# Kernel tuning notes

Measured on AMD Instinct MI355X. Metric: run time of the kernel, lower is better.

Reference implementation:

```python
import jax, jax.numpy as jnp
import numpy as np

B, S, D, H = 2, 2048, 1024, 16
DK = D // H


def setup_inputs() -> dict:
    key = jax.random.key(0)
    ks = jax.random.split(key, 12)
    scale = 1.0 / np.sqrt(D)
    inp = {
        "query": jax.random.normal(ks[0], (B, S, D), jnp.float32),
        "key": jax.random.normal(ks[1], (B, S, D), jnp.float32),
        "value": jax.random.normal(ks[2], (B, S, D), jnp.float32),
        "mask": jax.random.randint(ks[3], (B, 1, S, S), 0, 2, jnp.int32),
        "Wq": jax.random.normal(ks[4], (D, D), jnp.float32) * scale,
        "bq": jnp.zeros((D,), jnp.float32),
        "Wk": jax.random.normal(ks[5], (D, D), jnp.float32) * scale,
        "bk": jnp.zeros((D,), jnp.float32),
        "Wv": jax.random.normal(ks[6], (D, D), jnp.float32) * scale,
        "bv": jnp.zeros((D,), jnp.float32),
        "Wo": jax.random.normal(ks[7], (D, D), jnp.float32) * scale,
        "bo": jnp.zeros((D,), jnp.float32),
    }
    return inp


def reference(query, key, value, mask, Wq, bq, Wk, bk, Wv, bv, Wo, bo):
    # Linear projections (dropout is identity in eval mode)
    q = query @ Wq + bq          # (B,S,D)
    k = key @ Wk + bk
    v = value @ Wv + bv

    # split heads: (B,S,D) -> (B,H,S,DK)
    def split(x):
        return x.reshape(B, S, H, DK).transpose(0, 2, 1, 3)

    q, k, v = split(q), split(k), split(v)

    scores = jnp.einsum("bhqd,bhkd->bhqk", q, k) / jnp.sqrt(jnp.float32(DK))
    scores = jnp.where(mask == 0, jnp.float32(-1e9), scores)
    p_attn = jax.nn.softmax(scores, axis=-1)   # (B,H,S,S)

    att = jnp.einsum("bhqk,bhkd->bhqd", p_attn, v)  # (B,H,S,DK)
    merged = att.transpose(0, 2, 1, 3).reshape(B, S, D)
    return merged @ Wo + bo
```

## Files before the change

### kernel.cpp

```cpp
#include <hip/hip_runtime.h>
#include <hip/hip_bf16.h>
#include <cstdint>
#include <cstddef>


#define B_ 2
#define S_ 2048
#define D_ 1024
#define H_ 16
#define M_ 4096

typedef unsigned short u16;
typedef __attribute__((ext_vector_type(8))) short bf16x8;
typedef __attribute__((ext_vector_type(8))) unsigned short u16x8;
typedef __attribute__((ext_vector_type(4))) unsigned short u16x4;
typedef __attribute__((ext_vector_type(4))) unsigned int u32x4;
typedef __attribute__((ext_vector_type(4))) float f32x4;
typedef __attribute__((ext_vector_type(4))) int i32x4;

#define QSCALE 0.18033688011112042f

__device__ __forceinline__ u16 f2bf(float f) {
  __hip_bfloat16 h = __float2bfloat16(f);
  return *reinterpret_cast<u16*>(&h);
}

__device__ __forceinline__ unsigned cvtpk(float lo, float hi) {
  unsigned r;
  asm("v_cvt_pk_bf16_f32 %0, %1, %2" : "=v"(r) : "v"(lo), "v"(hi));
  return r;
}

__device__ __forceinline__ void gload_lds16(const void* g, void* l) {
  __builtin_amdgcn_global_load_lds((const __attribute__((address_space(1))) void*)g,
                                   (__attribute__((address_space(3))) void*)l, 16, 0, 0);
}

__global__ __launch_bounds__(256) void k_prep(const float* __restrict__ q, const float* __restrict__ k,
                                              const float* __restrict__ v,
                                              u16* __restrict__ xq, u16* __restrict__ xk, u16* __restrict__ xv,
                                              const float* __restrict__ w0, const float* __restrict__ w1,
                                              const float* __restrict__ w2, const float* __restrict__ w3,
                                              u16* __restrict__ t0, u16* __restrict__ t1,
                                              u16* __restrict__ t2, u16* __restrict__ t3,
                                              const int* __restrict__ mask, u16* __restrict__ mout) {
  __shared__ float tile[32][33];
  const int id = blockIdx.x;
  const int tid = threadIdx.x;
  if (id < 6144) {
    const int z = id >> 11;
    const int bx = id & 2047;
    const float* src = (z == 0) ? q : (z == 1) ? k : v;
    u16* dst = (z == 0) ? xq : (z == 1) ? xk : xv;
    size_t i = ((size_t)bx * 256 + tid) * 8;
    f32x4 a = *(const f32x4*)(src + i);
    f32x4 b = *(const f32x4*)(src + i + 4);
    u16x8 o;
    o[0]=f2bf(a[0]); o[1]=f2bf(a[1]); o[2]=f2bf(a[2]); o[3]=f2bf(a[3]);
    o[4]=f2bf(b[0]); o[5]=f2bf(b[1]); o[6]=f2bf(b[2]); o[7]=f2bf(b[3]);
    *(u16x8*)(dst + i) = o;
  } else if (id < 10240) {
    const int id2 = id - 6144;
    const int z = id2 >> 10;
    const int rem = id2 & 1023;
    const int bx0 = (rem & 31) * 32, by0 = (rem >> 5) * 32;
    const float* W = (z==0)?w0:(z==1)?w1:(z==2)?w2:w3;
    u16* Wt = (z==0)?t0:(z==1)?t1:(z==2)?t2:t3;
    int tx = tid & 31, ty = tid >> 5;
    #pragma unroll
    for (int p = 0; p < 4; ++p)
      tile[ty + p*8][tx] = W[(size_t)(by0 + ty + p*8) * D_ + bx0 + tx];
    __syncthreads();
    #pragma unroll
    for (int p = 0; p < 4; ++p)
      Wt[(size_t)(bx0 + ty + p*8) * D_ + by0 + tx] = f2bf(tile[tx][ty + p*8]);
  } else {
    size_t tt = (size_t)(id - 10240) * 256 + tid;
    const int* p = mask + tt * 64;
    unsigned wds0 = 0, wds1 = 0, wds2 = 0, wds3 = 0;
    #pragma unroll
    for (int c = 0; c < 16; ++c) {
      i32x4 vv = *(const i32x4*)(p + c*4);
      #pragma unroll
      for (int e = 0; e < 4; ++e) {
        const int kk = c*4 + e;
        const int lcw = (kk >> 3) & 3;
        const int ni = ((kk >> 4) & 2) | ((kk >> 2) & 1);
        const unsigned bit = 1u << (4*ni + (kk & 3));
        if (vv[e]) {
          if (lcw == 0) wds0 |= bit; else if (lcw == 1) wds1 |= bit;
          else if (lcw == 2) wds2 |= bit; else wds3 |= bit;
        }
      }
    }
    u16x4 w; w[0] = (u16)wds0; w[1] = (u16)wds1; w[2] = (u16)wds2; w[3] = (u16)wds3;
    *(u16x4*)(mout + tt*4) = w;
  }
}

template<int CMODE, int MI, int NI>
__device__ __forceinline__ void gemm_core(const u16* __restrict__ A, const u16* __restrict__ Bt,
                                          const float* __restrict__ bias, void* __restrict__ Cv, float scale) {
  extern __shared__ u16 sm[];
  constexpr int ASZ = MI*32*64;
  u16* As = sm;
  u16* Bs = sm + ASZ;
  const int t = threadIdx.x;
  const int l = t & 63, w = t >> 6;
  const int wr = w >> 1, wc = w & 1;
  const int lr = l & 15, lc = l >> 4;
  const int bm = blockIdx.x, bn = blockIdx.y;
  f32x4 acc[MI][NI];
  #pragma unroll
  for (int i = 0; i < MI; ++i)
    #pragma unroll
    for (int j = 0; j < NI; ++j) { f32x4 z = {0.f,0.f,0.f,0.f}; acc[i][j] = z; }
  const int srow = t >> 3;
  const int blkx = (t & 7) ^ (srow & 7);
  const u16* ga = A  + (size_t)(bm*(MI*32) + srow)*1024 + blkx*8;
  const u16* gb = Bt + (size_t)(bn*(NI*32) + srow)*1024 + blkx*8;
  for (int kt = 0; kt < 16; ++kt) {
    const int ko = kt * 64;
    __syncthreads();
    #pragma unroll
    for (int i = 0; i < MI; ++i)
      gload_lds16(ga + (size_t)(i*32)*1024 + ko, &As[i*2048 + t*8]);
    #pragma unroll
    for (int i = 0; i < NI; ++i)
      gload_lds16(gb + (size_t)(i*32)*1024 + ko, &Bs[i*2048 + t*8]);
    __syncthreads();
    #pragma unroll
    for (int ks = 0; ks < 2; ++ks) {
      bf16x8 af[MI], bfr[NI];
      #pragma unroll
      for (int mi = 0; mi < MI; ++mi)
        af[mi]  = *(const bf16x8*)&As[(wr*(MI*16) + mi*16 + lr)*64 + (((ks*4 + lc) ^ (lr & 7))*8)];
      #pragma unroll
      for (int ni = 0; ni < NI; ++ni)
        bfr[ni] = *(const bf16x8*)&Bs[(wc*(NI*16) + ni*16 + lr)*64 + (((ks*4 + lc) ^ (lr & 7))*8)];
      #pragma unroll
      for (int mi = 0; mi < MI; ++mi)
        #pragma unroll
        for (int ni = 0; ni < NI; ++ni)
          acc[mi][ni] = __builtin_amdgcn_mfma_f32_16x16x32_bf16(af[mi], bfr[ni], acc[mi][ni], 0, 0, 0);
    }
  }
  #pragma unroll
  for (int ni = 0; ni < NI; ++ni) {
    int gcol = bn*(NI*32) + wc*(NI*16) + ni*16 + lr;
    float bv = bias[gcol];
    #pragma unroll
    for (int mi = 0; mi < MI; ++mi) {
      int grow = bm*(MI*32) + wr*(MI*16) + mi*16 + lc*4;
      if (CMODE == 2) {
        u16x4 pk;
        #pragma unroll
        for (int j = 0; j < 4; ++j) pk[j] = f2bf((acc[mi][ni][j] + bv) * scale);
        *(u16x4*)&((u16*)Cv)[(size_t)gcol * M_ + grow] = pk;
      } else {
        #pragma unroll
        for (int j = 0; j < 4; ++j) {
          float v = (acc[mi][ni][j] + bv) * scale;
          if (CMODE == 0) ((u16*)Cv)[(size_t)(grow + j) * 1024 + gcol] = f2bf(v);
          else            ((float*)Cv)[(size_t)(grow + j) * 1024 + gcol] = v;
        }
      }
    }
  }
}

__global__ __launch_bounds__(256, 4) void k_gemm_qkv(const u16* Xq, const u16* Xk, const u16* Xv,
                                                     const u16* Wqt, const u16* Wkt, const u16* Wvt,
                                                     const float* bq, const float* bk, const float* bv,
                                                     u16* Qo, u16* Ko, u16* Vt, float qscale) {
  int z = blockIdx.z;
  if (z == 0)      gemm_core<0,4,4>(Xq, Wqt, bq, Qo, qscale);
  else if (z == 1) gemm_core<0,4,4>(Xk, Wkt, bk, Ko, 1.f);
  else             gemm_core<2,4,4>(Xv, Wvt, bv, Vt, 1.f);
}

__global__ __launch_bounds__(256, 4) void k_gemm_out(const u16* Aatt, const u16* Wot, const float* bo, float* out) {
  gemm_core<1,4,2>(Aatt, Wot, bo, out, 1.f);
}

__global__ __launch_bounds__(512, 4) void k_attn(const u16* __restrict__ Q, const u16* __restrict__ Kb,
                                                 const u16* __restrict__ Vt,
                                                 const u16* __restrict__ mbw,
                                                 u16* __restrict__ attb) {
  __shared__ u16 Ks[4*4096];
  __shared__ u16 Vs[4*4096];
  const int t = threadIdx.x, l = t & 63, w = t >> 6;
  const int lr = l & 15, lc = l >> 4;
  const int id = blockIdx.x + (blockIdx.y << 4) + (blockIdx.z << 8);
  const int lg = (id & 7) * 64 + (id >> 3);
  const int qt = lg & 15, h = (lg >> 4) & 15, b = lg >> 8;
  const int r0 = t >> 3;
  const int c0 = (t & 7) ^ (r0 & 7);
  const int pr0 = (r0 & 32) | ((r0 & 12) << 1) | ((r0 & 16) >> 2) | (r0 & 3);
  const u16* kp0 = Kb + (size_t)(b*S_ + pr0)*D_ + h*64 + c0*8;
  const u16* vp0 = Vt + (size_t)(h*64 + r0)*M_ + b*S_ + c0*8;

  gload_lds16(Q + (size_t)(b*S_ + qt*128 + r0)*D_      + h*64 + c0*8, &Ks[t*8]);
  gload_lds16(Q + (size_t)(b*S_ + qt*128 + 64 + r0)*D_ + h*64 + c0*8, &Ks[4096 + t*8]);
  __syncthreads();
  const int qrow = w*16 + lr;
  const int sw0 = ((lc     ) ^ (lr & 7)) * 8;
  const int sw1 = ((4 + lc ) ^ (lr & 7)) * 8;
  const int qbuf = (qrow >> 6) * 4096, qrl = (qrow & 63) * 64;
  bf16x8 aq0 = *(const bf16x8*)&Ks[qbuf + qrl + sw0];
  bf16x8 aq1 = *(const bf16x8*)&Ks[qbuf + qrl + sw1];
  __syncthreads();
  gload_lds16(kp0,                  &Ks[t*8]);
  gload_lds16(vp0,                  &Vs[t*8]);
  gload_lds16(kp0 + (size_t)64*D_,  &Ks[4096 + t*8]);
  gload_lds16(vp0 + 64,             &Vs[4096 + t*8]);

  const short one_bf = (short)0x3F80;
  const bf16x8 onesf = {one_bf,one_bf,one_bf,one_bf,one_bf,one_bf,one_bf,one_bf};
  f32x4 ls = {0.f,0.f,0.f,0.f};
  f32x4 o[4];
  #pragma unroll
  for (int ni = 0; ni < 4; ++ni) { f32x4 z = {0.f,0.f,0.f,0.f}; o[ni] = z; }
  const u16* mkp = mbw + (size_t)(b*S_ + qt*128 + qrow)*128 + lc;
  const u16* kpp = kp0;
  const u16* vpp = vp0;

#define ATILE(MN, SL) {                                                                \
    unsigned mw = mkp[(MN)*4];                                                         \
    f32x4 s[4];                                                                        \
    _Pragma("unroll")                                                                  \
    for (int ni = 0; ni < 4; ++ni) { f32x4 z = {0.f,0.f,0.f,0.f}; s[ni] = z; }         \
    __builtin_amdgcn_s_setprio(1);                                                     \
    _Pragma("unroll")                                                                  \
    for (int ni = 0; ni < 4; ++ni) {                                                   \
      bf16x8 bk0 = *(const bf16x8*)&Ks[(SL)*4096 + (ni*16 + lr)*64 + sw0];             \
      bf16x8 bk1 = *(const bf16x8*)&Ks[(SL)*4096 + (ni*16 + lr)*64 + sw1];             \
      s[ni] = __builtin_amdgcn_mfma_f32_16x16x32_bf16(bk0, aq0, s[ni], 0, 0, 0);       \
      s[ni] = __builtin_amdgcn_mfma_f32_16x16x32_bf16(bk1, aq1, s[ni], 0, 0, 0);       \
    }                                                                                  \
    __builtin_amdgcn_s_setprio(0);                                                     \
    _Pragma("unroll")                                                                  \
    for (int ni = 0; ni < 4; ++ni)                                                     \
      _Pragma("unroll")                                                                \
      for (int j = 0; j < 4; ++j) {                                                    \
        float pv = __builtin_amdgcn_exp2f(s[ni][j]);                                   \
        int bmsk = ((int)(mw << (31 - (4*ni + j)))) >> 31;                             \
        union { float f; int i; } u; u.f = pv; u.i &= bmsk;                            \
        s[ni][j] = u.f;                                                                \
      }                                                                                \
    u32x4 pw0, pw1;                                                                    \
    pw0[0] = cvtpk(s[0][0], s[0][1]); pw0[1] = cvtpk(s[0][2], s[0][3]);                \
    pw0[2] = cvtpk(s[1][0], s[1][1]); pw0[3] = cvtpk(s[1][2], s[1][3]);                \
    pw1[0] = cvtpk(s[2][0], s[2][1]); pw1[1] = cvtpk(s[2][2], s[2][3]);                \
    pw1[2] = cvtpk(s[3][0], s[3][1]); pw1[3] = cvtpk(s[3][2], s[3][3]);                \
    bf16x8 pa0 = __builtin_bit_cast(bf16x8, pw0);                                      \
    bf16x8 pa1 = __builtin_bit_cast(bf16x8, pw1);                                      \
    __builtin_amdgcn_s_setprio(1);                                                     \
    ls = __builtin_amdgcn_mfma_f32_16x16x32_bf16(pa0, onesf, ls, 0, 0, 0);             \
    ls = __builtin_amdgcn_mfma_f32_16x16x32_bf16(pa1, onesf, ls, 0, 0, 0);             \
    _Pragma("unroll")                                                                  \
    for (int ni = 0; ni < 4; ++ni) {                                                   \
      bf16x8 bv0 = *(const bf16x8*)&Vs[(SL)*4096 + (ni*16 + lr)*64 + sw0];             \
      o[ni] = __builtin_amdgcn_mfma_f32_16x16x32_bf16(pa0, bv0, o[ni], 0, 0, 0);       \
    }                                                                                  \
    _Pragma("unroll")                                                                  \
    for (int ni = 0; ni < 4; ++ni) {                                                   \
      bf16x8 bv1 = *(const bf16x8*)&Vs[(SL)*4096 + (ni*16 + lr)*64 + sw1];             \
      o[ni] = __builtin_amdgcn_mfma_f32_16x16x32_bf16(pa1, bv1, o[ni], 0, 0, 0);       \
    }                                                                                  \
    __builtin_amdgcn_s_setprio(0);                                                     \
  }

#define APHASE(PC, PRE) {                                                              \
    __syncthreads();                                                                   \
    if (PRE) {                                                                         \
      gload_lds16(kpp + (size_t)2*64*D_, &Ks[((1-(PC))*2    )*4096 + t*8]);            \
      gload_lds16(vpp + 2*64,            &Vs[((1-(PC))*2    )*4096 + t*8]);            \
      gload_lds16(kpp + (size_t)3*64*D_, &Ks[((1-(PC))*2 + 1)*4096 + t*8]);            \
      gload_lds16(vpp + 3*64,            &Vs[((1-(PC))*2 + 1)*4096 + t*8]);            \
    }                                                                                  \
    ATILE(0, (PC)*2);                                                                  \
    ATILE(1, (PC)*2 + 1);                                                              \
    kpp += (size_t)2*64*D_; vpp += 2*64; mkp += 8;                                     \
  }

  for (int it = 0; it < 7; ++it) {
    APHASE(0, 1)
    APHASE(1, 1)
  }
  APHASE(0, 1)
  APHASE(1, 0)
#undef APHASE
#undef ATILE

  float rl[4];
  #pragma unroll
  for (int j = 0; j < 4; ++j) rl[j] = 1.f / ls[j];
  #pragma unroll
  for (int ni = 0; ni < 4; ++ni)
    #pragma unroll
    for (int j = 0; j < 4; ++j) {
      int orow = qt*128 + w*16 + lc*4 + j, dcol = ni*16 + lr;
      attb[(size_t)(b*S_ + orow)*D_ + h*64 + dcol] = f2bf(o[ni][j] * rl[j]);
    }
}

extern "C" void kernel_launch(void* const* d_in, const int* in_sizes, int n_in,
                              void* d_out, int out_size, void* d_ws, size_t ws_size,
                              hipStream_t stream) {
  (void)in_sizes; (void)n_in; (void)out_size; (void)ws_size;
  const float* query = (const float*)d_in[0];
  const float* key   = (const float*)d_in[1];
  const float* value = (const float*)d_in[2];
  const int*   mask  = (const int*)d_in[3];
  const float* Wq = (const float*)d_in[4];
  const float* bq = (const float*)d_in[5];
  const float* Wk = (const float*)d_in[6];
  const float* bk = (const float*)d_in[7];
  const float* Wv = (const float*)d_in[8];
  const float* bv = (const float*)d_in[9];
  const float* Wo = (const float*)d_in[10];
  const float* bo = (const float*)d_in[11];
  float* out = (float*)d_out;
  char* ws = (char*)d_ws;
  const size_t MB = 1024 * 1024;
  u16* Xq  = (u16*)(ws + 0*MB);
  u16* Xk  = (u16*)(ws + 8*MB);
  u16* Xv  = (u16*)(ws + 16*MB);
  u16* Wqt = (u16*)(ws + 24*MB);
  u16* Wkt = (u16*)(ws + 26*MB);
  u16* Wvt = (u16*)(ws + 28*MB);
  u16* Wot = (u16*)(ws + 30*MB);
  u16* Qb  = (u16*)(ws + 32*MB);
  u16* Kb  = (u16*)(ws + 40*MB);
  u16* Vtb = (u16*)(ws + 48*MB);
  u16* mbits = (u16*)(ws + 56*MB);
  u16* attb = (u16*)(ws + 0*MB);

  k_prep     <<<dim3(10752),       256, 0,     stream>>>(query, key, value, Xq, Xk, Xv,
                                                         Wq, Wk, Wv, Wo, Wqt, Wkt, Wvt, Wot,
                                                         mask, mbits);
  k_gemm_qkv <<<dim3(32, 8, 3),    256, 32768, stream>>>(Xq, Xk, Xv, Wqt, Wkt, Wvt, bq, bk, bv,
                                                         Qb, Kb, Vtb, QSCALE);
  k_attn     <<<dim3(16, 16, 2),   512, 0,     stream>>>(Qb, Kb, Vtb, mbits, attb);
  k_gemm_out <<<dim3(32, 16),      256, 24576, stream>>>(attb, Wot, bo, out);
}
```

Baseline: 133.3 us.

## Split attention key range across two warp groups with 64-row query tiles

The attention kernel now processes 64 query rows per block instead of 128, doubling the grid. The key dimension is split between two groups of four waves, each handling half the keys in 32-key steps, and the partial outputs and row sums are combined through LDS at the end. The mask bit packing is simplified to a plain 64-bit word per row chunk, read one byte per step. This is meant to raise parallelism and cut per-wave serial latency, at the cost of an LDS reduction, smaller tiles per step and extra barriers.

```diff
diff --git a/kernel.cpp b/kernel.cpp
--- a/kernel.cpp
+++ b/kernel.cpp
@@ -11,6 +11,7 @@
 #define M_ 4096
 
 typedef unsigned short u16;
+typedef unsigned char u8;
 typedef __attribute__((ext_vector_type(8))) short bf16x8;
 typedef __attribute__((ext_vector_type(8))) unsigned short u16x8;
 typedef __attribute__((ext_vector_type(4))) unsigned short u16x4;
@@ -43,7 +44,7 @@
                                               const float* __restrict__ w2, const float* __restrict__ w3,
                                               u16* __restrict__ t0, u16* __restrict__ t1,
                                               u16* __restrict__ t2, u16* __restrict__ t3,
-                                              const int* __restrict__ mask, u16* __restrict__ mout) {
+                                              const int* __restrict__ mask, unsigned long long* __restrict__ mout) {
   __shared__ float tile[32][33];
   const int id = blockIdx.x;
   const int tid = threadIdx.x;
@@ -77,24 +78,15 @@
   } else {
     size_t tt = (size_t)(id - 10240) * 256 + tid;
     const int* p = mask + tt * 64;
-    unsigned wds0 = 0, wds1 = 0, wds2 = 0, wds3 = 0;
+    unsigned long long bits = 0ull;
     #pragma unroll
     for (int c = 0; c < 16; ++c) {
       i32x4 vv = *(const i32x4*)(p + c*4);
       #pragma unroll
-      for (int e = 0; e < 4; ++e) {
-        const int kk = c*4 + e;
-        const int lcw = (kk >> 3) & 3;
-        const int ni = ((kk >> 4) & 2) | ((kk >> 2) & 1);
-        const unsigned bit = 1u << (4*ni + (kk & 3));
-        if (vv[e]) {
-          if (lcw == 0) wds0 |= bit; else if (lcw == 1) wds1 |= bit;
-          else if (lcw == 2) wds2 |= bit; else wds3 |= bit;
-        }
-      }
+      for (int e = 0; e < 4; ++e)
+        if (vv[e]) bits |= 1ull << (c*4 + e);
     }
-    u16x4 w; w[0] = (u16)wds0; w[1] = (u16)wds1; w[2] = (u16)wds2; w[3] = (u16)wds3;
-    *(u16x4*)(mout + tt*4) = w;
+    mout[tt] = bits;
   }
 }
 
@@ -185,35 +177,40 @@
 
 __global__ __launch_bounds__(512, 4) void k_attn(const u16* __restrict__ Q, const u16* __restrict__ Kb,
                                                  const u16* __restrict__ Vt,
-                                                 const u16* __restrict__ mbw,
+                                                 const u8* __restrict__ mbw,
                                                  u16* __restrict__ attb) {
-  __shared__ u16 Ks[4*4096];
-  __shared__ u16 Vs[4*4096];
+  __shared__ u16 smem[16384];
+  u16* Ks = smem;
+  u16* Vs = smem + 8192;
   const int t = threadIdx.x, l = t & 63, w = t >> 6;
   const int lr = l & 15, lc = l >> 4;
-  const int id = blockIdx.x + (blockIdx.y << 4) + (blockIdx.z << 8);
-  const int lg = (id & 7) * 64 + (id >> 3);
-  const int qt = lg & 15, h = (lg >> 4) & 15, b = lg >> 8;
-  const int r0 = t >> 3;
-  const int c0 = (t & 7) ^ (r0 & 7);
-  const int pr0 = (r0 & 32) | ((r0 & 12) << 1) | ((r0 & 16) >> 2) | (r0 & 3);
-  const u16* kp0 = Kb + (size_t)(b*S_ + pr0)*D_ + h*64 + c0*8;
-  const u16* vp0 = Vt + (size_t)(h*64 + r0)*M_ + b*S_ + c0*8;
-
-  gload_lds16(Q + (size_t)(b*S_ + qt*128 + r0)*D_      + h*64 + c0*8, &Ks[t*8]);
-  gload_lds16(Q + (size_t)(b*S_ + qt*128 + 64 + r0)*D_ + h*64 + c0*8, &Ks[4096 + t*8]);
+  const int g = w >> 2;
+  const int wq = w & 3;
+  const int id = blockIdx.x + (blockIdx.y << 5) + (blockIdx.z << 9);
+  const int lg = (id & 7) * 128 + (id >> 3);
+  const int qt = lg & 31, h = (lg >> 5) & 15, b = lg >> 9;
+  const int u = t & 255;
+  const int kr = u >> 3;
+  const int kc = (u & 7) ^ (kr & 7);
+  const int kpr = ((kr & 12) << 1) | ((kr & 16) >> 2) | (kr & 3);
+  const u16* kp = Kb + ((size_t)(b*S_ + g*1024 + kpr))*D_ + h*64 + kc*8;
+  const int vr = u >> 2;
+  const int vc = (u & 3) ^ (vr & 3);
+  const u16* vp = Vt + ((size_t)(h*64 + vr))*M_ + b*S_ + g*1024 + vc*8;
+
+  {
+    int qr = t >> 3, qc = (t & 7) ^ (qr & 7);
+    gload_lds16(Q + (size_t)(b*S_ + qt*64 + qr)*D_ + h*64 + qc*8, &smem[t*8]);
+  }
   __syncthreads();
-  const int qrow = w*16 + lr;
   const int sw0 = ((lc     ) ^ (lr & 7)) * 8;
   const int sw1 = ((4 + lc ) ^ (lr & 7)) * 8;
-  const int qbuf = (qrow >> 6) * 4096, qrl = (qrow & 63) * 64;
-  bf16x8 aq0 = *(const bf16x8*)&Ks[qbuf + qrl + sw0];
-  bf16x8 aq1 = *(const bf16x8*)&Ks[qbuf + qrl + sw1];
+  const int qrow = wq*16 + lr;
+  bf16x8 aq0 = *(const bf16x8*)&smem[qrow*64 + sw0];
+  bf16x8 aq1 = *(const bf16x8*)&smem[qrow*64 + sw1];
   __syncthreads();
-  gload_lds16(kp0,                  &Ks[t*8]);
-  gload_lds16(vp0,                  &Vs[t*8]);
-  gload_lds16(kp0 + (size_t)64*D_,  &Ks[4096 + t*8]);
-  gload_lds16(vp0 + 64,             &Vs[4096 + t*8]);
+  gload_lds16(kp, &Ks[(g*2)*2048 + u*8]);
+  gload_lds16(vp, &Vs[(g*2)*2048 + u*8]);
 
   const short one_bf = (short)0x3F80;
   const bf16x8 onesf = {one_bf,one_bf,one_bf,one_bf,one_bf,one_bf,one_bf,one_bf};
@@ -221,88 +218,95 @@
   f32x4 o[4];
   #pragma unroll
   for (int ni = 0; ni < 4; ++ni) { f32x4 z = {0.f,0.f,0.f,0.f}; o[ni] = z; }
-  const u16* mkp = mbw + (size_t)(b*S_ + qt*128 + qrow)*128 + lc;
-  const u16* kpp = kp0;
-  const u16* vpp = vp0;
-
-#define ATILE(MN, SL) {                                                                \
-    unsigned mw = mkp[(MN)*4];                                                         \
-    f32x4 s[4];                                                                        \
-    _Pragma("unroll")                                                                  \
-    for (int ni = 0; ni < 4; ++ni) { f32x4 z = {0.f,0.f,0.f,0.f}; s[ni] = z; }         \
+  const u16* kpp = kp;
+  const u16* vpp = vp;
+  const u8* mkp = mbw + (size_t)(b*S_ + qt*64 + qrow)*256 + g*128 + lc;
+  const int vsw = (lc ^ (lr & 3)) * 8;
+
+#define APH(P, PRE) {                                                                  \
+    __syncthreads();                                                                   \
+    unsigned mw = (unsigned)(*mkp);                                                    \
+    if (PRE) {                                                                         \
+      gload_lds16(kpp + (size_t)32*D_, &Ks[(g*2 + ((P)^1))*2048 + u*8]);               \
+      gload_lds16(vpp + 32,            &Vs[(g*2 + ((P)^1))*2048 + u*8]);               \
+    }                                                                                  \
+    f32x4 s0 = {0.f,0.f,0.f,0.f}, s1 = {0.f,0.f,0.f,0.f};                              \
     __builtin_amdgcn_s_setprio(1);                                                     \
-    _Pragma("unroll")                                                                  \
-    for (int ni = 0; ni < 4; ++ni) {                                                   \
-      bf16x8 bk0 = *(const bf16x8*)&Ks[(SL)*4096 + (ni*16 + lr)*64 + sw0];             \
-      bf16x8 bk1 = *(const bf16x8*)&Ks[(SL)*4096 + (ni*16 + lr)*64 + sw1];             \
-      s[ni] = __builtin_amdgcn_mfma_f32_16x16x32_bf16(bk0, aq0, s[ni], 0, 0, 0);       \
-      s[ni] = __builtin_amdgcn_mfma_f32_16x16x32_bf16(bk1, aq1, s[ni], 0, 0, 0);       \
+    {                                                                                  \
+      const int kb = (g*2 + (P))*2048;                                                 \
+      bf16x8 bk00 = *(const bf16x8*)&Ks[kb + lr*64 + sw0];                             \
+      bf16x8 bk01 = *(const bf16x8*)&Ks[kb + lr*64 + sw1];                             \
+      bf16x8 bk10 = *(const bf16x8*)&Ks[kb + (16 + lr)*64 + sw0];                      \
+      bf16x8 bk11 = *(const bf16x8*)&Ks[kb + (16 + lr)*64 + sw1];                      \
+      s0 = __builtin_amdgcn_mfma_f32_16x16x32_bf16(bk00, aq0, s0, 0, 0, 0);            \
+      s0 = __builtin_amdgcn_mfma_f32_16x16x32_bf16(bk01, aq1, s0, 0, 0, 0);            \
+      s1 = __builtin_amdgcn_mfma_f32_16x16x32_bf16(bk10, aq0, s1, 0, 0, 0);            \
+      s1 = __builtin_amdgcn_mfma_f32_16x16x32_bf16(bk11, aq1, s1, 0, 0, 0);            \
     }                                                                                  \
     __builtin_amdgcn_s_setprio(0);                                                     \
     _Pragma("unroll")                                                                  \
-    for (int ni = 0; ni < 4; ++ni)                                                     \
+    for (int j = 0; j < 4; ++j) {                                                      \
+      float pv = __builtin_amdgcn_exp2f(s0[j]);                                        \
+      int bm0 = ((int)(mw << (31 - j))) >> 31;                                         \
+      union { float f; int i; } u0; u0.f = pv; u0.i &= bm0; s0[j] = u0.f;              \
+      float pw = __builtin_amdgcn_exp2f(s1[j]);                                        \
+      int bm1 = ((int)(mw << (27 - j))) >> 31;                                         \
+      union { float f; int i; } u1; u1.f = pw; u1.i &= bm1; s1[j] = u1.f;              \
+    }                                                                                  \
+    u32x4 pw4;                                                                         \
+    pw4[0] = cvtpk(s0[0], s0[1]); pw4[1] = cvtpk(s0[2], s0[3]);                        \
+    pw4[2] = cvtpk(s1[0], s1[1]); pw4[3] = cvtpk(s1[2], s1[3]);                        \
+    bf16x8 pa = __builtin_bit_cast(bf16x8, pw4);                                       \
+    __builtin_amdgcn_s_setprio(1);                                                     \
+    ls = __builtin_amdgcn_mfma_f32_16x16x32_bf16(pa, onesf, ls, 0, 0, 0);              \
+    {                                                                                  \
+      const int vb = (g*2 + (P))*2048;                                                 \
       _Pragma("unroll")                                                                \
-      for (int j = 0; j < 4; ++j) {                                                    \
-        float pv = __builtin_amdgcn_exp2f(s[ni][j]);                                   \
-        int bmsk = ((int)(mw << (31 - (4*ni + j)))) >> 31;                             \
-        union { float f; int i; } u; u.f = pv; u.i &= bmsk;                            \
-        s[ni][j] = u.f;                                                                \
+      for (int ni = 0; ni < 4; ++ni) {                                                 \
+        bf16x8 bv = *(const bf16x8*)&Vs[vb + (ni*16 + lr)*32 + vsw];                   \
+        o[ni] = __builtin_amdgcn_mfma_f32_16x16x32_bf16(pa, bv, o[ni], 0, 0, 0);       \
       }                                                                                \
-    u32x4 pw0, pw1;                                                                    \
-    pw0[0] = cvtpk(s[0][0], s[0][1]); pw0[1] = cvtpk(s[0][2], s[0][3]);                \
-    pw0[2] = cvtpk(s[1][0], s[1][1]); pw0[3] = cvtpk(s[1][2], s[1][3]);                \
-    pw1[0] = cvtpk(s[2][0], s[2][1]); pw1[1] = cvtpk(s[2][2], s[2][3]);                \
-    pw1[2] = cvtpk(s[3][0], s[3][1]); pw1[3] = cvtpk(s[3][2], s[3][3]);                \
-    bf16x8 pa0 = __builtin_bit_cast(bf16x8, pw0);                                      \
-    bf16x8 pa1 = __builtin_bit_cast(bf16x8, pw1);                                      \
-    __builtin_amdgcn_s_setprio(1);                                                     \
-    ls = __builtin_amdgcn_mfma_f32_16x16x32_bf16(pa0, onesf, ls, 0, 0, 0);             \
-    ls = __builtin_amdgcn_mfma_f32_16x16x32_bf16(pa1, onesf, ls, 0, 0, 0);             \
-    _Pragma("unroll")                                                                  \
-    for (int ni = 0; ni < 4; ++ni) {                                                   \
-      bf16x8 bv0 = *(const bf16x8*)&Vs[(SL)*4096 + (ni*16 + lr)*64 + sw0];             \
-      o[ni] = __builtin_amdgcn_mfma_f32_16x16x32_bf16(pa0, bv0, o[ni], 0, 0, 0);       \
-    }                                                                                  \
-    _Pragma("unroll")                                                                  \
-    for (int ni = 0; ni < 4; ++ni) {                                                   \
-      bf16x8 bv1 = *(const bf16x8*)&Vs[(SL)*4096 + (ni*16 + lr)*64 + sw1];             \
-      o[ni] = __builtin_amdgcn_mfma_f32_16x16x32_bf16(pa1, bv1, o[ni], 0, 0, 0);       \
     }                                                                                  \
     __builtin_amdgcn_s_setprio(0);                                                     \
-  }
-
-#define APHASE(PC, PRE) {                                                              \
-    __syncthreads();                                                                   \
-    if (PRE) {                                                                         \
-      gload_lds16(kpp + (size_t)2*64*D_, &Ks[((1-(PC))*2    )*4096 + t*8]);            \
-      gload_lds16(vpp + 2*64,            &Vs[((1-(PC))*2    )*4096 + t*8]);            \
-      gload_lds16(kpp + (size_t)3*64*D_, &Ks[((1-(PC))*2 + 1)*4096 + t*8]);            \
-      gload_lds16(vpp + 3*64,            &Vs[((1-(PC))*2 + 1)*4096 + t*8]);            \
-    }                                                                                  \
-    ATILE(0, (PC)*2);                                                                  \
-    ATILE(1, (PC)*2 + 1);                                                              \
-    kpp += (size_t)2*64*D_; vpp += 2*64; mkp += 8;                                     \
-  }
-
-  for (int it = 0; it < 7; ++it) {
-    APHASE(0, 1)
-    APHASE(1, 1)
-  }
-  APHASE(0, 1)
-  APHASE(1, 0)
-#undef APHASE
-#undef ATILE
-
-  float rl[4];
-  #pragma unroll
-  for (int j = 0; j < 4; ++j) rl[j] = 1.f / ls[j];
-  #pragma unroll
-  for (int ni = 0; ni < 4; ++ni)
-    #pragma unroll
-    for (int j = 0; j < 4; ++j) {
-      int orow = qt*128 + w*16 + lc*4 + j, dcol = ni*16 + lr;
-      attb[(size_t)(b*S_ + orow)*D_ + h*64 + dcol] = f2bf(o[ni][j] * rl[j]);
-    }
+    kpp += (size_t)32*D_; vpp += 32; mkp += 4;                                         \
+  }
+
+  for (int it = 0; it < 15; ++it) {
+    APH(0, 1)
+    APH(1, 1)
+  }
+  APH(0, 1)
+  APH(1, 0)
+#undef APH
+
+  __syncthreads();
+  float* cm = (float*)smem;
+  const int idx = (wq*64 + l) * 20;
+  if (g == 1) {
+    *(f32x4*)&cm[idx]      = o[0];
+    *(f32x4*)&cm[idx + 4]  = o[1];
+    *(f32x4*)&cm[idx + 8]  = o[2];
+    *(f32x4*)&cm[idx + 12] = o[3];
+    *(f32x4*)&cm[idx + 16] = ls;
+  }
+  __syncthreads();
+  if (g == 0) {
+    o[0] += *(const f32x4*)&cm[idx];
+    o[1] += *(const f32x4*)&cm[idx + 4];
+    o[2] += *(const f32x4*)&cm[idx + 8];
+    o[3] += *(const f32x4*)&cm[idx + 12];
+    ls   += *(const f32x4*)&cm[idx + 16];
+    float rl[4];
+    #pragma unroll
+    for (int j = 0; j < 4; ++j) rl[j] = 1.f / ls[j];
+    #pragma unroll
+    for (int ni = 0; ni < 4; ++ni)
+      #pragma unroll
+      for (int j = 0; j < 4; ++j) {
+        int orow = qt*64 + wq*16 + lc*4 + j, dcol = ni*16 + lr;
+        attb[(size_t)(b*S_ + orow)*D_ + h*64 + dcol] = f2bf(o[ni][j] * rl[j]);
+      }
+  }
 }
 
 extern "C" void kernel_launch(void* const* d_in, const int* in_sizes, int n_in,
@@ -334,7 +338,7 @@
   u16* Qb  = (u16*)(ws + 32*MB);
   u16* Kb  = (u16*)(ws + 40*MB);
   u16* Vtb = (u16*)(ws + 48*MB);
-  u16* mbits = (u16*)(ws + 56*MB);
+  unsigned long long* mbits = (unsigned long long*)(ws + 56*MB);
   u16* attb = (u16*)(ws + 0*MB);
 
   k_prep     <<<dim3(10752),       256, 0,     stream>>>(query, key, value, Xq, Xk, Xv,
@@ -342,6 +346,6 @@
                                                          mask, mbits);
   k_gemm_qkv <<<dim3(32, 8, 3),    256, 32768, stream>>>(Xq, Xk, Xv, Wqt, Wkt, Wvt, bq, bk, bv,
                                                          Qb, Kb, Vtb, QSCALE);
-  k_attn     <<<dim3(16, 16, 2),   512, 0,     stream>>>(Qb, Kb, Vtb, mbits, attb);
+  k_attn     <<<dim3(32, 16, 2),   512, 0,     stream>>>(Qb, Kb, Vtb, (const u8*)mbits, attb);
   k_gemm_out <<<dim3(32, 16),      256, 24576, stream>>>(attb, Wot, bo, out);
 }
```

Result: slower. 152.9 us (+14.7%).
